# Kernel tuning notes

Hardware: AMD Instinct MI355X
Metric: run time of the kernel (lower is better)

## Reference

```python
import jax, jax.numpy as jnp
import numpy as np

HEAD_NUM = 7
HEAD_DIM = 64
HIDDEN = 896

def rotate_half(t):
    d = t.shape[-1] // 2
    return jnp.concatenate([-t[..., d:], t[..., :d]], axis=-1)

def setup_inputs() -> dict:
    key = jax.random.key(0)
    ks = jax.random.split(key, 11)
    B, S = 4, 2048
    proj = HEAD_NUM * HEAD_DIM  # 448
    sc_in = 1.0 / np.sqrt(HIDDEN)
    sc_pr = 1.0 / np.sqrt(proj)
    pos = jnp.arange(S)[:, None].astype(jnp.float32)
    inv_freq = 1.0 / (10000.0 ** (jnp.arange(0, HEAD_DIM, 2, dtype=jnp.float32) / HEAD_DIM))
    ang = pos * inv_freq[None, :]              # [S, D/2]
    emb = jnp.concatenate([ang, ang], axis=-1) # [S, D]
    return {
        'x': jax.random.normal(ks[0], (B, S, HIDDEN), jnp.float32),
        'cos': jnp.cos(emb),
        'sin': jnp.sin(emb),
        'q_w': jax.random.normal(ks[1], (proj, HIDDEN), jnp.float32) * sc_in,
        'q_b': jax.random.normal(ks[2], (proj,), jnp.float32) * 0.01,
        'k_w': jax.random.normal(ks[3], (proj, HIDDEN), jnp.float32) * sc_in,
        'k_b': jax.random.normal(ks[4], (proj,), jnp.float32) * 0.01,
        'v_w': jax.random.normal(ks[5], (proj, HIDDEN), jnp.float32) * sc_in,
        'v_b': jax.random.normal(ks[6], (proj,), jnp.float32) * 0.01,
        'o_w': jax.random.normal(ks[7], (HIDDEN, proj), jnp.float32) * sc_pr,
        'o_b': jax.random.normal(ks[8], (HIDDEN,), jnp.float32) * 0.01,
    }

def reference(x, cos, sin, q_w, q_b, k_w, k_b, v_w, v_b, o_w, o_b):
    B, S, _ = x.shape
    def proj(w, b):
        y = jnp.einsum('bsh,ph->bsp', x, w) + b          # [B,S,H*D]
        return y.reshape(B, S, HEAD_NUM, HEAD_DIM).transpose(0, 2, 1, 3)  # [B,H,S,D]
    q = proj(q_w, q_b)
    k = proj(k_w, k_b)
    v = proj(v_w, v_b)
    c = cos[None, None, :, :]
    s = sin[None, None, :, :]
    q = q * c + rotate_half(q) * s
    k = k * c + rotate_half(k) * s
    scores = jnp.einsum('bhqd,bhkd->bhqk', q, k) / np.sqrt(HEAD_DIM)
    attn = jax.nn.softmax(scores, axis=-1)
    out = jnp.einsum('bhqk,bhkd->bhqd', attn, v)          # [B,H,S,D]
    out = out.transpose(0, 2, 1, 3).reshape(B, S, HEAD_NUM * HEAD_DIM)
    return jnp.einsum('bsp,hp->bsh', out, o_w) + o_b
```

## Files before the change

### kernel.cpp

```cpp
#include <hip/hip_runtime.h>

typedef _Float16 f16;
typedef __attribute__((ext_vector_type(8))) _Float16 f16x8;
typedef __attribute__((ext_vector_type(4))) _Float16 f16x4;
typedef __attribute__((ext_vector_type(4))) float f32x4;

#define MFMA(a,b,c) __builtin_amdgcn_mfma_f32_16x16x32_f16(a,b,c,0,0,0)

constexpr int HN = 7, HD = 64, HID = 896, PR = 448;
constexpr int NB = 4, NS = 2048, NM = NB * NS;
constexpr float LOG2E = 1.44269504088896f;

__device__ __forceinline__ void gload16(const f16* g, f16* l) {
    __builtin_amdgcn_global_load_lds(
        (const __attribute__((address_space(1))) void*)g,
        (__attribute__((address_space(3))) void*)l,
        16, 0, 0);
}

__device__ __forceinline__ int xcd_swz(int orig, int per) {
    return (orig & 7) * per + (orig >> 3);
}

__global__ __launch_bounds__(256) void conv_kernel(
    const float* __restrict__ x,  const float* __restrict__ qw,
    const float* __restrict__ kw, const float* __restrict__ vw,
    const float* __restrict__ ow,
    f16* __restrict__ xb, f16* __restrict__ wq, f16* __restrict__ wk,
    f16* __restrict__ wv, f16* __restrict__ wo)
{
    const int XV = NM * HID / 4;
    const int WV = PR * HID / 4;
    const int TOT = XV + 4 * WV;
    int64_t stride = (int64_t)gridDim.x * blockDim.x;
    for (int64_t v = (int64_t)blockIdx.x * 256 + threadIdx.x; v < TOT; v += stride) {
        const float* src; f16* dst; int64_t off;
        if (v < XV)               { src = x;  dst = xb; off = v; }
        else if (v < XV + WV)     { src = qw; dst = wq; off = v - XV; }
        else if (v < XV + 2*WV)   { src = kw; dst = wk; off = v - XV - WV; }
        else if (v < XV + 3*WV)   { src = vw; dst = wv; off = v - XV - 2*WV; }
        else                      { src = ow; dst = wo; off = v - XV - 3*WV; }
        f32x4 fv = *((const f32x4*)src + off);
        f16x4 hv = { (f16)fv[0], (f16)fv[1], (f16)fv[2], (f16)fv[3] };
        *((f16x4*)dst + off) = hv;
    }
}

__global__ __launch_bounds__(256) void qkv_gemm(
    const f16* __restrict__ xb, const f16* __restrict__ wq,
    const f16* __restrict__ wk, const f16* __restrict__ wv,
    const float* __restrict__ qb, const float* __restrict__ kb,
    const float* __restrict__ vb,
    const float* __restrict__ cosT, const float* __restrict__ sinT,
    f16* __restrict__ Q, f16* __restrict__ K, f16* __restrict__ Vt)
{
    extern __shared__ char smem[];
    f16* As = (f16*)smem;
    f16* Bs = (f16*)(smem + 256*64*2);
    f16* Cs = (f16*)smem;

    const int wg = xcd_swz(blockIdx.x, 84);
    const int tynt = wg % 21, mt = wg / 21;
    const int ty = tynt / 7, nt = tynt % 7;
    const int m0 = mt * 256, n0 = nt * 64;

    const f16* w = (ty == 0) ? wq : (ty == 1) ? wk : wv;
    const float* bias = (ty == 0) ? qb : (ty == 1) ? kb : vb;

    const int tid = threadIdx.x;
    const int wv_ = tid >> 6, lane = tid & 63;
    const int g = lane >> 4, lr = lane & 15;
    const int lrow = lane >> 3;
    const int cswz = (lane & 7) ^ (lrow & 7);

    const int ch0 = ((0*4 + g) ^ (lr & 7)) * 8;
    const int ch1 = ((1*4 + g) ^ (lr & 7)) * 8;

    f32x4 acc[4][4] = {};

    for (int k0 = 0; k0 < HID; k0 += 64) {
        #pragma unroll
        for (int p = 0; p < 8; p++) {
            int rt = wv_*64 + p*8;
            gload16(xb + (int64_t)(m0 + rt + lrow)*HID + k0 + cswz*8, As + rt*64);
        }
        #pragma unroll
        for (int p = 0; p < 2; p++) {
            int rt = wv_*16 + p*8;
            gload16(w + (int64_t)(n0 + rt + lrow)*HID + k0 + cswz*8, Bs + rt*64);
        }
        __syncthreads();
        #pragma unroll
        for (int kc = 0; kc < 2; kc++) {
            const int ch = kc ? ch1 : ch0;
            f16x8 af[4], bf[4];
            #pragma unroll
            for (int fm = 0; fm < 4; fm++)
                af[fm] = *(const f16x8*)(As + (wv_*64 + fm*16 + lr)*64 + ch);
            #pragma unroll
            for (int fn = 0; fn < 4; fn++)
                bf[fn] = *(const f16x8*)(Bs + (fn*16 + lr)*64 + ch);
            #pragma unroll
            for (int fm = 0; fm < 4; fm++)
                #pragma unroll
                for (int fn = 0; fn < 4; fn++)
                    acc[fm][fn] = MFMA(af[fm], bf[fn], acc[fm][fn]);
        }
        __syncthreads();
    }

    float bias_f[4];
    #pragma unroll
    for (int fn = 0; fn < 4; fn++) bias_f[fn] = bias[n0 + fn*16 + lr];
    #pragma unroll
    for (int fm = 0; fm < 4; fm++)
        #pragma unroll
        for (int fn = 0; fn < 4; fn++)
            #pragma unroll
            for (int j = 0; j < 4; j++)
                Cs[(wv_*64 + fm*16 + g*4 + j)*72 + fn*16 + lr] = (f16)(acc[fm][fn][j] + bias_f[fn]);
    __syncthreads();

    const int b = m0 / NS;
    const int s0 = m0 % NS;
    const int64_t bhbase = ((int64_t)(b*HN + nt)) * NS * HD;

    if (ty < 2) {
        const float scale = (ty == 0) ? 0.125f * LOG2E : 1.0f;
        const int r = tid, s = s0 + r;
        const f16* crow = Cs + r*72;
        const float* cr = cosT + s*64;
        const float* sr = sinT + s*64;
        f16 vals[64];
        #pragma unroll
        for (int i = 0; i < 4; i++) {
            f16x8 ylo = *(const f16x8*)(crow + i*8);
            f16x8 yhi = *(const f16x8*)(crow + 32 + i*8);
            #pragma unroll
            for (int h = 0; h < 2; h++) {
                f32x4 cl = *(const f32x4*)(cr + i*8 + h*4);
                f32x4 sl = *(const f32x4*)(sr + i*8 + h*4);
                f32x4 chh = *(const f32x4*)(cr + 32 + i*8 + h*4);
                f32x4 shh = *(const f32x4*)(sr + 32 + i*8 + h*4);
                #pragma unroll
                for (int j = 0; j < 4; j++) {
                    float lo = (float)ylo[h*4+j], hi = (float)yhi[h*4+j];
                    vals[i*8 + h*4 + j]      = (f16)((lo*cl[j] - hi*sl[j]) * scale);
                    vals[32 + i*8 + h*4 + j] = (f16)((hi*chh[j] + lo*shh[j]) * scale);
                }
            }
        }
        if (ty == 0) {
            f16* p = Q + bhbase + (int64_t)s * HD;
            #pragma unroll
            for (int i = 0; i < 8; i++)
                *(f16x8*)(p + i*8) = *(f16x8*)(vals + i*8);
        } else {
            int tt = (s0 >> 6) + (r >> 6);
            int rt = r & 63;
            f16* base = K + bhbase + tt*4096 + rt*64;
            #pragma unroll
            for (int i = 0; i < 8; i++)
                *(f16x8*)(base + (i ^ (rt & 7))*8) = *(f16x8*)(vals + i*8);
        }
    } else {
        const int d = tid & 63, sblk = tid >> 6, si0 = sblk * 64;
        f16 vals[64];
        #pragma unroll
        for (int i = 0; i < 64; i++)
            vals[i] = Cs[(si0 + i)*72 + d];
        int tt = (s0 >> 6) + sblk;
        f16* base = Vt + bhbase + tt*4096 + d*64;
        #pragma unroll
        for (int i = 0; i < 8; i++)
            *(f16x8*)(base + (i ^ (d & 7))*8) = *(f16x8*)(vals + i*8);
    }
}

__global__ __launch_bounds__(256) void attn_kernel(
    const f16* __restrict__ Q, const f16* __restrict__ K2,
    const f16* __restrict__ V2, f16* __restrict__ O)
{
    __shared__ __align__(16) f16 KVs[2][2][4096];
    __shared__ __align__(16) f16 Pl[4][16][72];

    const int wg = xcd_swz(blockIdx.x, 112);
    const int qb = wg % 32, bh = wg / 32;
    const int tid = threadIdx.x, w = tid >> 6, lane = tid & 63;
    const int g = lane >> 4, lr = lane & 15;
    const int q0 = qb * 64 + w * 16;

    const int64_t bhoff = (int64_t)bh * NS * HD;
    const f16* Qp = Q + bhoff;
    const f16* Kp = K2 + bhoff;
    const f16* Vp = V2 + bhoff;

    f16x8 aq0 = *(const f16x8*)(Qp + (q0 + lr) * HD + g * 8);
    f16x8 aq1 = *(const f16x8*)(Qp + (q0 + lr) * HD + 32 + g * 8);

    const int stoff = w * 1024 + lane * 8;
    const int ldoff = w * 1024;

    gload16(Kp + stoff,       &KVs[0][0][ldoff]);
    gload16(Kp + stoff + 512, &KVs[0][0][ldoff + 512]);
    gload16(Vp + stoff,       &KVs[0][1][ldoff]);
    gload16(Vp + stoff + 512, &KVs[0][1][ldoff + 512]);
    __syncthreads();

    f32x4 accO[4] = {};
    float mrun = -1e30f, srun = 0.f;

    const int ch0 = (g ^ (lr & 7)) * 8;
    const int ch1 = ((4 + g) ^ (lr & 7)) * 8;

    int buf = 0;
    for (int t = 0; t < NS / 64; ++t) {
        if (t + 1 < NS / 64) {
            const f16* ks = Kp + (t + 1) * 4096 + stoff;
            const f16* vs = Vp + (t + 1) * 4096 + stoff;
            gload16(ks,       &KVs[buf ^ 1][0][ldoff]);
            gload16(ks + 512, &KVs[buf ^ 1][0][ldoff + 512]);
            gload16(vs,       &KVs[buf ^ 1][1][ldoff]);
            gload16(vs + 512, &KVs[buf ^ 1][1][ldoff + 512]);
        }
        const f16* Ks = &KVs[buf][0][0];
        const f16* Vs = &KVs[buf][1][0];

        f32x4 sf[4];
        __builtin_amdgcn_s_setprio(1);
        #pragma unroll
        for (int kt = 0; kt < 4; ++kt) {
            const f16* kl = Ks + (kt * 16 + lr) * 64;
            f16x8 k0 = *(const f16x8*)(kl + ch0);
            f16x8 k1 = *(const f16x8*)(kl + ch1);
            f32x4 z = {};
            z = MFMA(k0, aq0, z);
            z = MFMA(k1, aq1, z);
            sf[kt] = z;
        }
        __builtin_amdgcn_s_setprio(0);

        float m0a = fmaxf(fmaxf(sf[0][0], sf[0][1]), fmaxf(sf[0][2], sf[0][3]));
        float m1a = fmaxf(fmaxf(sf[1][0], sf[1][1]), fmaxf(sf[1][2], sf[1][3]));
        float m2a = fmaxf(fmaxf(sf[2][0], sf[2][1]), fmaxf(sf[2][2], sf[2][3]));
        float m3a = fmaxf(fmaxf(sf[3][0], sf[3][1]), fmaxf(sf[3][2], sf[3][3]));
        float pmax = fmaxf(fmaxf(m0a, m1a), fmaxf(m2a, m3a));
        pmax = fmaxf(pmax, __shfl_xor(pmax, 16, 64));
        pmax = fmaxf(pmax, __shfl_xor(pmax, 32, 64));

        if (!__all(pmax - mrun <= 8.0f)) {
            float mn = fmaxf(mrun, pmax);
            float corr = exp2f(mrun - mn);
            mrun = mn;
            srun *= corr;
            #pragma unroll
            for (int fn = 0; fn < 4; ++fn)
                #pragma unroll
                for (int j = 0; j < 4; ++j)
                    accO[fn][j] *= corr;
        }

        float pf[16];
        #pragma unroll
        for (int kt = 0; kt < 4; ++kt)
            #pragma unroll
            for (int j = 0; j < 4; ++j)
                pf[kt*4 + j] = exp2f(sf[kt][j] - mrun);

        float s0a = (pf[0] + pf[1]) + (pf[2] + pf[3]);
        float s1a = (pf[4] + pf[5]) + (pf[6] + pf[7]);
        float s2a = (pf[8] + pf[9]) + (pf[10] + pf[11]);
        float s3a = (pf[12] + pf[13]) + (pf[14] + pf[15]);
        float tsum = (s0a + s1a) + (s2a + s3a);
        tsum += __shfl_xor(tsum, 16, 64);
        tsum += __shfl_xor(tsum, 32, 64);
        srun += tsum;

        #pragma unroll
        for (int kt = 0; kt < 4; ++kt) {
            f16x4 pk = { (f16)pf[kt*4+0], (f16)pf[kt*4+1], (f16)pf[kt*4+2], (f16)pf[kt*4+3] };
            *(f16x4*)&Pl[w][lr][kt*16 + g*4] = pk;
        }
        f16x8 p0 = *(const f16x8*)&Pl[w][lr][g * 8];
        f16x8 p1 = *(const f16x8*)&Pl[w][lr][32 + g * 8];

        __builtin_amdgcn_s_setprio(1);
        #pragma unroll
        for (int fn = 0; fn < 4; ++fn) {
            const f16* vl = Vs + (fn * 16 + lr) * 64;
            f16x8 v0 = *(const f16x8*)(vl + ch0);
            f16x8 v1 = *(const f16x8*)(vl + ch1);
            accO[fn] = MFMA(v0, p0, accO[fn]);
            accO[fn] = MFMA(v1, p1, accO[fn]);
        }
        __builtin_amdgcn_s_setprio(0);
        __syncthreads();
        buf ^= 1;
    }

    const int b = bh / HN, h = bh % HN;
    const float inv = 1.0f / srun;
    const int q = q0 + lr;
    f16* orow = O + ((int64_t)b * NS + q) * PR + h * HD;
    #pragma unroll
    for (int fn = 0; fn < 4; ++fn) {
        f16x4 hv = { (f16)(accO[fn][0] * inv), (f16)(accO[fn][1] * inv),
                     (f16)(accO[fn][2] * inv), (f16)(accO[fn][3] * inv) };
        *(f16x4*)(orow + fn * 16 + g * 4) = hv;
    }
}

__global__ __launch_bounds__(256) void oproj_gemm(
    const f16* __restrict__ Ob, const f16* __restrict__ wo,
    const float* __restrict__ ob, float* __restrict__ out)
{
    extern __shared__ char smem[];
    f16* As = (f16*)smem;
    f16* Bs = (f16*)(smem + 128*64*2);

    const int wg = xcd_swz(blockIdx.x, 56);
    const int nt = wg % 7, mt = wg / 7;
    const int m0 = mt*128, n0 = nt*128;
    const int tid = threadIdx.x;
    const int wv_ = tid >> 6, lane = tid & 63;
    const int wm = wv_ >> 1, wn = wv_ & 1;
    const int g = lane >> 4, lr = lane & 15;
    const int lrow = lane >> 3;
    const int cswz = (lane & 7) ^ (lrow & 7);

    const int ch0 = (g ^ (lr & 7)) * 8;
    const int ch1 = ((4 + g) ^ (lr & 7)) * 8;

    f32x4 acc[4][4] = {};

    for (int k0 = 0; k0 < PR; k0 += 64) {
        #pragma unroll
        for (int p = 0; p < 4; p++) {
            int rt = wv_*32 + p*8;
            gload16(Ob + (int64_t)(m0 + rt + lrow)*PR + k0 + cswz*8, As + rt*64);
        }
        #pragma unroll
        for (int p = 0; p < 4; p++) {
            int rt = wv_*32 + p*8;
            gload16(wo + (int64_t)(n0 + rt + lrow)*PR + k0 + cswz*8, Bs + rt*64);
        }
        __syncthreads();
        #pragma unroll
        for (int kc = 0; kc < 2; kc++) {
            const int ch = kc ? ch1 : ch0;
            f16x8 af[4], bf[4];
            #pragma unroll
            for (int fm = 0; fm < 4; fm++)
                af[fm] = *(const f16x8*)(As + (wm*64 + fm*16 + lr)*64 + ch);
            #pragma unroll
            for (int fn = 0; fn < 4; fn++)
                bf[fn] = *(const f16x8*)(Bs + (wn*64 + fn*16 + lr)*64 + ch);
            #pragma unroll
            for (int fm = 0; fm < 4; fm++)
                #pragma unroll
                for (int fn = 0; fn < 4; fn++)
                    acc[fm][fn] = MFMA(af[fm], bf[fn], acc[fm][fn]);
        }
        __syncthreads();
    }

    float bias_f[4];
    #pragma unroll
    for (int fn = 0; fn < 4; fn++) bias_f[fn] = ob[n0 + wn*64 + fn*16 + lr];
    #pragma unroll
    for (int fm = 0; fm < 4; fm++)
        #pragma unroll
        for (int fn = 0; fn < 4; fn++)
            #pragma unroll
            for (int j = 0; j < 4; j++) {
                int row = m0 + wm*64 + fm*16 + g*4 + j;
                int col = n0 + wn*64 + fn*16 + lr;
                out[(int64_t)row*HID + col] = acc[fm][fn][j] + bias_f[fn];
            }
}

extern "C" void kernel_launch(void* const* d_in, const int* in_sizes, int n_in,
                              void* d_out, int out_size, void* d_ws, size_t ws_size,
                              hipStream_t stream) {
    const float* x    = (const float*)d_in[0];
    const float* cosT = (const float*)d_in[1];
    const float* sinT = (const float*)d_in[2];
    const float* qw   = (const float*)d_in[3];
    const float* qb   = (const float*)d_in[4];
    const float* kw   = (const float*)d_in[5];
    const float* kb   = (const float*)d_in[6];
    const float* vw   = (const float*)d_in[7];
    const float* vb   = (const float*)d_in[8];
    const float* ow   = (const float*)d_in[9];
    const float* ob   = (const float*)d_in[10];
    float* out = (float*)d_out;

    char* ws = (char*)d_ws;
    f16* xb = (f16*)ws;  ws += (size_t)NM * HID * 2;
    f16* wqf = (f16*)ws; ws += (size_t)PR * HID * 2;
    f16* wkf = (f16*)ws; ws += (size_t)PR * HID * 2;
    f16* wvf = (f16*)ws; ws += (size_t)PR * HID * 2;
    f16* wof = (f16*)ws; ws += (size_t)HID * PR * 2;
    f16* Qb = (f16*)ws;  ws += (size_t)NB * HN * NS * HD * 2;
    f16* Kb = (f16*)ws;  ws += (size_t)NB * HN * NS * HD * 2;
    f16* Vt = (f16*)ws;  ws += (size_t)NB * HN * HD * NS * 2;
    f16* Obuf = (f16*)ws; ws += (size_t)NM * PR * 2;

    conv_kernel<<<dim3(2048), dim3(256), 0, stream>>>(x, qw, kw, vw, ow, xb, wqf, wkf, wvf, wof);
    qkv_gemm<<<dim3(672), dim3(256), 40960, stream>>>(xb, wqf, wkf, wvf, qb, kb, vb, cosT, sinT, Qb, Kb, Vt);
    attn_kernel<<<dim3(896), dim3(256), 0, stream>>>(Qb, Kb, Vt, Obuf);
    oproj_gemm<<<dim3(448), dim3(256), 32768, stream>>>(Obuf, wof, ob, out);
}
```

Measured before the change: 254.5 us.

## Retile QKV and O-proj GEMMs smaller; process 32 queries per warp in attention

The QKV GEMM moves from 256x64 to 128x64 tiles (1344 blocks) and the output projection from 128x128 to 128x64 tiles (896 blocks), with the RoPE and V-transpose epilogues split across two threads per row. The attention kernel now handles 128 queries per block (32 per warp as two 16-row halves), so each K/V tile loaded into LDS feeds twice as many MFMAs, and the P staging buffer gets an XOR swizzle. The intent is better occupancy and wave balance for the GEMMs, and less K/V traffic per query in attention. The trade-off is more register pressure in attention and only 448 attention blocks, which may underfill the GPU.

```diff
diff --git a/kernel.cpp b/kernel.cpp
--- a/kernel.cpp
+++ b/kernel.cpp
@@ -56,32 +56,33 @@
 {
     extern __shared__ char smem[];
     f16* As = (f16*)smem;
-    f16* Bs = (f16*)(smem + 256*64*2);
+    f16* Bs = (f16*)(smem + 128*64*2);
     f16* Cs = (f16*)smem;
 
-    const int wg = xcd_swz(blockIdx.x, 84);
+    const int wg = xcd_swz(blockIdx.x, 168);
     const int tynt = wg % 21, mt = wg / 21;
     const int ty = tynt / 7, nt = tynt % 7;
-    const int m0 = mt * 256, n0 = nt * 64;
+    const int m0 = mt * 128, n0 = nt * 64;
 
     const f16* w = (ty == 0) ? wq : (ty == 1) ? wk : wv;
     const float* bias = (ty == 0) ? qb : (ty == 1) ? kb : vb;
 
     const int tid = threadIdx.x;
     const int wv_ = tid >> 6, lane = tid & 63;
+    const int wm = wv_ >> 1, wn = wv_ & 1;
     const int g = lane >> 4, lr = lane & 15;
     const int lrow = lane >> 3;
     const int cswz = (lane & 7) ^ (lrow & 7);
 
-    const int ch0 = ((0*4 + g) ^ (lr & 7)) * 8;
-    const int ch1 = ((1*4 + g) ^ (lr & 7)) * 8;
-
-    f32x4 acc[4][4] = {};
+    const int ch0 = (g ^ (lr & 7)) * 8;
+    const int ch1 = ((4 + g) ^ (lr & 7)) * 8;
+
+    f32x4 acc[4][2] = {};
 
     for (int k0 = 0; k0 < HID; k0 += 64) {
         #pragma unroll
-        for (int p = 0; p < 8; p++) {
-            int rt = wv_*64 + p*8;
+        for (int p = 0; p < 4; p++) {
+            int rt = wv_*32 + p*8;
             gload16(xb + (int64_t)(m0 + rt + lrow)*HID + k0 + cswz*8, As + rt*64);
         }
         #pragma unroll
@@ -93,32 +94,32 @@
         #pragma unroll
         for (int kc = 0; kc < 2; kc++) {
             const int ch = kc ? ch1 : ch0;
-            f16x8 af[4], bf[4];
+            f16x8 af[4], bf[2];
             #pragma unroll
             for (int fm = 0; fm < 4; fm++)
-                af[fm] = *(const f16x8*)(As + (wv_*64 + fm*16 + lr)*64 + ch);
-            #pragma unroll
-            for (int fn = 0; fn < 4; fn++)
-                bf[fn] = *(const f16x8*)(Bs + (fn*16 + lr)*64 + ch);
+                af[fm] = *(const f16x8*)(As + (wm*64 + fm*16 + lr)*64 + ch);
+            #pragma unroll
+            for (int fn = 0; fn < 2; fn++)
+                bf[fn] = *(const f16x8*)(Bs + (wn*32 + fn*16 + lr)*64 + ch);
             #pragma unroll
             for (int fm = 0; fm < 4; fm++)
                 #pragma unroll
-                for (int fn = 0; fn < 4; fn++)
+                for (int fn = 0; fn < 2; fn++)
                     acc[fm][fn] = MFMA(af[fm], bf[fn], acc[fm][fn]);
         }
         __syncthreads();
     }
 
-    float bias_f[4];
-    #pragma unroll
-    for (int fn = 0; fn < 4; fn++) bias_f[fn] = bias[n0 + fn*16 + lr];
+    float bias_f[2];
+    #pragma unroll
+    for (int fn = 0; fn < 2; fn++) bias_f[fn] = bias[n0 + wn*32 + fn*16 + lr];
     #pragma unroll
     for (int fm = 0; fm < 4; fm++)
         #pragma unroll
-        for (int fn = 0; fn < 4; fn++)
+        for (int fn = 0; fn < 2; fn++)
             #pragma unroll
             for (int j = 0; j < 4; j++)
-                Cs[(wv_*64 + fm*16 + g*4 + j)*72 + fn*16 + lr] = (f16)(acc[fm][fn][j] + bias_f[fn]);
+                Cs[(wm*64 + fm*16 + g*4 + j)*72 + wn*32 + fn*16 + lr] = (f16)(acc[fm][fn][j] + bias_f[fn]);
     __syncthreads();
 
     const int b = m0 / NS;
@@ -127,53 +128,57 @@
 
     if (ty < 2) {
         const float scale = (ty == 0) ? 0.125f * LOG2E : 1.0f;
-        const int r = tid, s = s0 + r;
+        const int r = tid >> 1, d0 = (tid & 1) * 32, s = s0 + r;
         const f16* crow = Cs + r*72;
-        const float* cr = cosT + s*64;
-        const float* sr = sinT + s*64;
-        f16 vals[64];
-        #pragma unroll
-        for (int i = 0; i < 4; i++) {
-            f16x8 ylo = *(const f16x8*)(crow + i*8);
-            f16x8 yhi = *(const f16x8*)(crow + 32 + i*8);
-            #pragma unroll
-            for (int h = 0; h < 2; h++) {
-                f32x4 cl = *(const f32x4*)(cr + i*8 + h*4);
-                f32x4 sl = *(const f32x4*)(sr + i*8 + h*4);
-                f32x4 chh = *(const f32x4*)(cr + 32 + i*8 + h*4);
-                f32x4 shh = *(const f32x4*)(sr + 32 + i*8 + h*4);
+        f16 vals[32];
+        if (d0 == 0) {
+            #pragma unroll
+            for (int i = 0; i < 8; i++) {
+                f32x4 cl = *(const f32x4*)(cosT + s*64 + i*4);
+                f32x4 sl = *(const f32x4*)(sinT + s*64 + i*4);
                 #pragma unroll
                 for (int j = 0; j < 4; j++) {
-                    float lo = (float)ylo[h*4+j], hi = (float)yhi[h*4+j];
-                    vals[i*8 + h*4 + j]      = (f16)((lo*cl[j] - hi*sl[j]) * scale);
-                    vals[32 + i*8 + h*4 + j] = (f16)((hi*chh[j] + lo*shh[j]) * scale);
+                    float lo = (float)crow[i*4+j], hi = (float)crow[32 + i*4+j];
+                    vals[i*4 + j] = (f16)((lo*cl[j] - hi*sl[j]) * scale);
                 }
             }
+        } else {
+            #pragma unroll
+            for (int i = 0; i < 8; i++) {
+                f32x4 cl = *(const f32x4*)(cosT + s*64 + 32 + i*4);
+                f32x4 sl = *(const f32x4*)(sinT + s*64 + 32 + i*4);
+                #pragma unroll
+                for (int j = 0; j < 4; j++) {
+                    float lo = (float)crow[i*4+j], hi = (float)crow[32 + i*4+j];
+                    vals[i*4 + j] = (f16)((hi*cl[j] + lo*sl[j]) * scale);
+                }
+            }
         }
         if (ty == 0) {
-            f16* p = Q + bhbase + (int64_t)s * HD;
-            #pragma unroll
-            for (int i = 0; i < 8; i++)
+            f16* p = Q + bhbase + (int64_t)s * HD + d0;
+            #pragma unroll
+            for (int i = 0; i < 4; i++)
                 *(f16x8*)(p + i*8) = *(f16x8*)(vals + i*8);
         } else {
             int tt = (s0 >> 6) + (r >> 6);
             int rt = r & 63;
             f16* base = K + bhbase + tt*4096 + rt*64;
             #pragma unroll
-            for (int i = 0; i < 8; i++)
-                *(f16x8*)(base + (i ^ (rt & 7))*8) = *(f16x8*)(vals + i*8);
+            for (int i = 0; i < 4; i++)
+                *(f16x8*)(base + (((d0>>3) + i) ^ (rt & 7))*8) = *(f16x8*)(vals + i*8);
         }
     } else {
-        const int d = tid & 63, sblk = tid >> 6, si0 = sblk * 64;
-        f16 vals[64];
-        #pragma unroll
-        for (int i = 0; i < 64; i++)
+        const int d = tid & 63, sblk = tid >> 6, si0 = sblk * 32;
+        f16 vals[32];
+        #pragma unroll
+        for (int i = 0; i < 32; i++)
             vals[i] = Cs[(si0 + i)*72 + d];
-        int tt = (s0 >> 6) + sblk;
+        int tt = (s0 >> 6) + (si0 >> 6);
+        int sb = si0 & 63;
         f16* base = Vt + bhbase + tt*4096 + d*64;
         #pragma unroll
-        for (int i = 0; i < 8; i++)
-            *(f16x8*)(base + (i ^ (d & 7))*8) = *(f16x8*)(vals + i*8);
+        for (int i = 0; i < 4; i++)
+            *(f16x8*)(base + (((sb>>3) + i) ^ (d & 7))*8) = *(f16x8*)(vals + i*8);
     }
 }
 
@@ -182,21 +187,25 @@
     const f16* __restrict__ V2, f16* __restrict__ O)
 {
     __shared__ __align__(16) f16 KVs[2][2][4096];
-    __shared__ __align__(16) f16 Pl[4][16][72];
-
-    const int wg = xcd_swz(blockIdx.x, 112);
-    const int qb = wg % 32, bh = wg / 32;
+    __shared__ __align__(16) f16 Pl[4][32][64];
+
+    const int wg = xcd_swz(blockIdx.x, 56);
+    const int qb = wg & 15, bh = wg >> 4;
     const int tid = threadIdx.x, w = tid >> 6, lane = tid & 63;
     const int g = lane >> 4, lr = lane & 15;
-    const int q0 = qb * 64 + w * 16;
+    const int q0 = qb * 128 + w * 32;
 
     const int64_t bhoff = (int64_t)bh * NS * HD;
     const f16* Qp = Q + bhoff;
     const f16* Kp = K2 + bhoff;
     const f16* Vp = V2 + bhoff;
 
-    f16x8 aq0 = *(const f16x8*)(Qp + (q0 + lr) * HD + g * 8);
-    f16x8 aq1 = *(const f16x8*)(Qp + (q0 + lr) * HD + 32 + g * 8);
+    f16x8 aq[2][2];
+    #pragma unroll
+    for (int qh = 0; qh < 2; qh++) {
+        aq[qh][0] = *(const f16x8*)(Qp + (q0 + qh*16 + lr) * HD + g * 8);
+        aq[qh][1] = *(const f16x8*)(Qp + (q0 + qh*16 + lr) * HD + 32 + g * 8);
+    }
 
     const int stoff = w * 1024 + lane * 8;
     const int ldoff = w * 1024;
@@ -207,11 +216,12 @@
     gload16(Vp + stoff + 512, &KVs[0][1][ldoff + 512]);
     __syncthreads();
 
-    f32x4 accO[4] = {};
-    float mrun = -1e30f, srun = 0.f;
+    f32x4 accO[2][4] = {};
+    float mrun[2] = {-1e30f, -1e30f}, srun[2] = {0.f, 0.f};
 
     const int ch0 = (g ^ (lr & 7)) * 8;
     const int ch1 = ((4 + g) ^ (lr & 7)) * 8;
+    const int pswz = (lr & 7) * 8;
 
     int buf = 0;
     for (int t = 0; t < NS / 64; ++t) {
@@ -226,63 +236,80 @@
         const f16* Ks = &KVs[buf][0][0];
         const f16* Vs = &KVs[buf][1][0];
 
-        f32x4 sf[4];
+        f32x4 sf[2][4];
         __builtin_amdgcn_s_setprio(1);
         #pragma unroll
         for (int kt = 0; kt < 4; ++kt) {
             const f16* kl = Ks + (kt * 16 + lr) * 64;
             f16x8 k0 = *(const f16x8*)(kl + ch0);
             f16x8 k1 = *(const f16x8*)(kl + ch1);
-            f32x4 z = {};
-            z = MFMA(k0, aq0, z);
-            z = MFMA(k1, aq1, z);
-            sf[kt] = z;
+            #pragma unroll
+            for (int qh = 0; qh < 2; ++qh) {
+                f32x4 z = {};
+                z = MFMA(k0, aq[qh][0], z);
+                z = MFMA(k1, aq[qh][1], z);
+                sf[qh][kt] = z;
+            }
         }
         __builtin_amdgcn_s_setprio(0);
 
-        float m0a = fmaxf(fmaxf(sf[0][0], sf[0][1]), fmaxf(sf[0][2], sf[0][3]));
-        float m1a = fmaxf(fmaxf(sf[1][0], sf[1][1]), fmaxf(sf[1][2], sf[1][3]));
-        float m2a = fmaxf(fmaxf(sf[2][0], sf[2][1]), fmaxf(sf[2][2], sf[2][3]));
-        float m3a = fmaxf(fmaxf(sf[3][0], sf[3][1]), fmaxf(sf[3][2], sf[3][3]));
-        float pmax = fmaxf(fmaxf(m0a, m1a), fmaxf(m2a, m3a));
-        pmax = fmaxf(pmax, __shfl_xor(pmax, 16, 64));
-        pmax = fmaxf(pmax, __shfl_xor(pmax, 32, 64));
-
-        if (!__all(pmax - mrun <= 8.0f)) {
-            float mn = fmaxf(mrun, pmax);
-            float corr = exp2f(mrun - mn);
-            mrun = mn;
-            srun *= corr;
-            #pragma unroll
-            for (int fn = 0; fn < 4; ++fn)
+        float pmax[2];
+        #pragma unroll
+        for (int qh = 0; qh < 2; ++qh) {
+            float m0a = fmaxf(fmaxf(sf[qh][0][0], sf[qh][0][1]), fmaxf(sf[qh][0][2], sf[qh][0][3]));
+            float m1a = fmaxf(fmaxf(sf[qh][1][0], sf[qh][1][1]), fmaxf(sf[qh][1][2], sf[qh][1][3]));
+            float m2a = fmaxf(fmaxf(sf[qh][2][0], sf[qh][2][1]), fmaxf(sf[qh][2][2], sf[qh][2][3]));
+            float m3a = fmaxf(fmaxf(sf[qh][3][0], sf[qh][3][1]), fmaxf(sf[qh][3][2], sf[qh][3][3]));
+            float pm = fmaxf(fmaxf(m0a, m1a), fmaxf(m2a, m3a));
+            pm = fmaxf(pm, __shfl_xor(pm, 16, 64));
+            pm = fmaxf(pm, __shfl_xor(pm, 32, 64));
+            pmax[qh] = pm;
+        }
+
+        if (!__all(pmax[0] - mrun[0] <= 8.0f && pmax[1] - mrun[1] <= 8.0f)) {
+            #pragma unroll
+            for (int qh = 0; qh < 2; ++qh) {
+                float mn = fmaxf(mrun[qh], pmax[qh]);
+                float corr = exp2f(mrun[qh] - mn);
+                mrun[qh] = mn;
+                srun[qh] *= corr;
+                #pragma unroll
+                for (int fn = 0; fn < 4; ++fn)
+                    #pragma unroll
+                    for (int j = 0; j < 4; ++j)
+                        accO[qh][fn][j] *= corr;
+            }
+        }
+
+        #pragma unroll
+        for (int qh = 0; qh < 2; ++qh) {
+            #pragma unroll
+            for (int kt = 0; kt < 4; ++kt)
                 #pragma unroll
                 for (int j = 0; j < 4; ++j)
-                    accO[fn][j] *= corr;
-        }
-
-        float pf[16];
-        #pragma unroll
-        for (int kt = 0; kt < 4; ++kt)
-            #pragma unroll
-            for (int j = 0; j < 4; ++j)
-                pf[kt*4 + j] = exp2f(sf[kt][j] - mrun);
-
-        float s0a = (pf[0] + pf[1]) + (pf[2] + pf[3]);
-        float s1a = (pf[4] + pf[5]) + (pf[6] + pf[7]);
-        float s2a = (pf[8] + pf[9]) + (pf[10] + pf[11]);
-        float s3a = (pf[12] + pf[13]) + (pf[14] + pf[15]);
-        float tsum = (s0a + s1a) + (s2a + s3a);
-        tsum += __shfl_xor(tsum, 16, 64);
-        tsum += __shfl_xor(tsum, 32, 64);
-        srun += tsum;
-
-        #pragma unroll
-        for (int kt = 0; kt < 4; ++kt) {
-            f16x4 pk = { (f16)pf[kt*4+0], (f16)pf[kt*4+1], (f16)pf[kt*4+2], (f16)pf[kt*4+3] };
-            *(f16x4*)&Pl[w][lr][kt*16 + g*4] = pk;
-        }
-        f16x8 p0 = *(const f16x8*)&Pl[w][lr][g * 8];
-        f16x8 p1 = *(const f16x8*)&Pl[w][lr][32 + g * 8];
+                    sf[qh][kt][j] = exp2f(sf[qh][kt][j] - mrun[qh]);
+            float s0a = (sf[qh][0][0] + sf[qh][0][1]) + (sf[qh][0][2] + sf[qh][0][3]);
+            float s1a = (sf[qh][1][0] + sf[qh][1][1]) + (sf[qh][1][2] + sf[qh][1][3]);
+            float s2a = (sf[qh][2][0] + sf[qh][2][1]) + (sf[qh][2][2] + sf[qh][2][3]);
+            float s3a = (sf[qh][3][0] + sf[qh][3][1]) + (sf[qh][3][2] + sf[qh][3][3]);
+            float tsum = (s0a + s1a) + (s2a + s3a);
+            tsum += __shfl_xor(tsum, 16, 64);
+            tsum += __shfl_xor(tsum, 32, 64);
+            srun[qh] += tsum;
+            #pragma unroll
+            for (int kt = 0; kt < 4; ++kt) {
+                f16x4 pk = { (f16)sf[qh][kt][0], (f16)sf[qh][kt][1],
+                             (f16)sf[qh][kt][2], (f16)sf[qh][kt][3] };
+                *(f16x4*)&Pl[w][qh*16 + lr][(kt*16 + g*4) ^ pswz] = pk;
+            }
+        }
+
+        f16x8 p0[2], p1[2];
+        #pragma unroll
+        for (int qh = 0; qh < 2; ++qh) {
+            p0[qh] = *(const f16x8*)&Pl[w][qh*16 + lr][ch0];
+            p1[qh] = *(const f16x8*)&Pl[w][qh*16 + lr][ch1];
+        }
 
         __builtin_amdgcn_s_setprio(1);
         #pragma unroll
@@ -290,8 +317,11 @@
             const f16* vl = Vs + (fn * 16 + lr) * 64;
             f16x8 v0 = *(const f16x8*)(vl + ch0);
             f16x8 v1 = *(const f16x8*)(vl + ch1);
-            accO[fn] = MFMA(v0, p0, accO[fn]);
-            accO[fn] = MFMA(v1, p1, accO[fn]);
+            #pragma unroll
+            for (int qh = 0; qh < 2; ++qh) {
+                accO[qh][fn] = MFMA(v0, p0[qh], accO[qh][fn]);
+                accO[qh][fn] = MFMA(v1, p1[qh], accO[qh][fn]);
+            }
         }
         __builtin_amdgcn_s_setprio(0);
         __syncthreads();
@@ -299,14 +329,17 @@
     }
 
     const int b = bh / HN, h = bh % HN;
-    const float inv = 1.0f / srun;
-    const int q = q0 + lr;
-    f16* orow = O + ((int64_t)b * NS + q) * PR + h * HD;
-    #pragma unroll
-    for (int fn = 0; fn < 4; ++fn) {
-        f16x4 hv = { (f16)(accO[fn][0] * inv), (f16)(accO[fn][1] * inv),
-                     (f16)(accO[fn][2] * inv), (f16)(accO[fn][3] * inv) };
-        *(f16x4*)(orow + fn * 16 + g * 4) = hv;
+    #pragma unroll
+    for (int qh = 0; qh < 2; ++qh) {
+        const float inv = 1.0f / srun[qh];
+        const int q = q0 + qh*16 + lr;
+        f16* orow = O + ((int64_t)b * NS + q) * PR + h * HD;
+        #pragma unroll
+        for (int fn = 0; fn < 4; ++fn) {
+            f16x4 hv = { (f16)(accO[qh][fn][0] * inv), (f16)(accO[qh][fn][1] * inv),
+                         (f16)(accO[qh][fn][2] * inv), (f16)(accO[qh][fn][3] * inv) };
+            *(f16x4*)(orow + fn * 16 + g * 4) = hv;
+        }
     }
 }
 
@@ -318,9 +351,9 @@
     f16* As = (f16*)smem;
     f16* Bs = (f16*)(smem + 128*64*2);
 
-    const int wg = xcd_swz(blockIdx.x, 56);
-    const int nt = wg % 7, mt = wg / 7;
-    const int m0 = mt*128, n0 = nt*128;
+    const int wg = xcd_swz(blockIdx.x, 112);
+    const int nt = wg % 14, mt = wg / 14;
+    const int m0 = mt*128, n0 = nt*64;
     const int tid = threadIdx.x;
     const int wv_ = tid >> 6, lane = tid & 63;
     const int wm = wv_ >> 1, wn = wv_ & 1;
@@ -331,7 +364,7 @@
     const int ch0 = (g ^ (lr & 7)) * 8;
     const int ch1 = ((4 + g) ^ (lr & 7)) * 8;
 
-    f32x4 acc[4][4] = {};
+    f32x4 acc[4][2] = {};
 
     for (int k0 = 0; k0 < PR; k0 += 64) {
         #pragma unroll
@@ -340,41 +373,41 @@
             gload16(Ob + (int64_t)(m0 + rt + lrow)*PR + k0 + cswz*8, As + rt*64);
         }
         #pragma unroll
-        for (int p = 0; p < 4; p++) {
-            int rt = wv_*32 + p*8;
+        for (int p = 0; p < 2; p++) {
+            int rt = wv_*16 + p*8;
             gload16(wo + (int64_t)(n0 + rt + lrow)*PR + k0 + cswz*8, Bs + rt*64);
         }
         __syncthreads();
         #pragma unroll
         for (int kc = 0; kc < 2; kc++) {
             const int ch = kc ? ch1 : ch0;
-            f16x8 af[4], bf[4];
+            f16x8 af[4], bf[2];
             #pragma unroll
             for (int fm = 0; fm < 4; fm++)
                 af[fm] = *(const f16x8*)(As + (wm*64 + fm*16 + lr)*64 + ch);
             #pragma unroll
-            for (int fn = 0; fn < 4; fn++)
-                bf[fn] = *(const f16x8*)(Bs + (wn*64 + fn*16 + lr)*64 + ch);
+            for (int fn = 0; fn < 2; fn++)
+                bf[fn] = *(const f16x8*)(Bs + (wn*32 + fn*16 + lr)*64 + ch);
             #pragma unroll
             for (int fm = 0; fm < 4; fm++)
                 #pragma unroll
-                for (int fn = 0; fn < 4; fn++)
+                for (int fn = 0; fn < 2; fn++)
                     acc[fm][fn] = MFMA(af[fm], bf[fn], acc[fm][fn]);
         }
         __syncthreads();
     }
 
-    float bias_f[4];
-    #pragma unroll
-    for (int fn = 0; fn < 4; fn++) bias_f[fn] = ob[n0 + wn*64 + fn*16 + lr];
+    float bias_f[2];
+    #pragma unroll
+    for (int fn = 0; fn < 2; fn++) bias_f[fn] = ob[n0 + wn*32 + fn*16 + lr];
     #pragma unroll
     for (int fm = 0; fm < 4; fm++)
         #pragma unroll
-        for (int fn = 0; fn < 4; fn++)
+        for (int fn = 0; fn < 2; fn++)
             #pragma unroll
             for (int j = 0; j < 4; j++) {
                 int row = m0 + wm*64 + fm*16 + g*4 + j;
-                int col = n0 + wn*64 + fn*16 + lr;
+                int col = n0 + wn*32 + fn*16 + lr;
                 out[(int64_t)row*HID + col] = acc[fm][fn][j] + bias_f[fn];
             }
 }
@@ -407,7 +440,7 @@
     f16* Obuf = (f16*)ws; ws += (size_t)NM * PR * 2;
 
     conv_kernel<<<dim3(2048), dim3(256), 0, stream>>>(x, qw, kw, vw, ow, xb, wqf, wkf, wvf, wof);
-    qkv_gemm<<<dim3(672), dim3(256), 40960, stream>>>(xb, wqf, wkf, wvf, qb, kb, vb, cosT, sinT, Qb, Kb, Vt);
-    attn_kernel<<<dim3(896), dim3(256), 0, stream>>>(Qb, Kb, Vt, Obuf);
-    oproj_gemm<<<dim3(448), dim3(256), 32768, stream>>>(Obuf, wof, ob, out);
-}
+    qkv_gemm<<<dim3(1344), dim3(256), 24576, stream>>>(xb, wqf, wkf, wvf, qb, kb, vb, cosT, sinT, Qb, Kb, Vt);
+    attn_kernel<<<dim3(448), dim3(256), 0, stream>>>(Qb, Kb, Vt, Obuf);
+    oproj_gemm<<<dim3(896), dim3(256), 24576, stream>>>(Obuf, wof, ob, out);
+}
```

New measurement: 222.6 us. 1.14x faster.
